# Optimization experiments

Hardware: AMD Instinct MI355X
Metric: run time of the kernel (lower is better)

The kernel has to match this reference:

```python
import jax, jax.numpy as jnp
import numpy as np

HEADS, LEVELS, POINTS, ZANCH = 8, 4, 8, 4
EMBED = 256
SHAPES = np.array([[92, 160], [46, 80], [23, 40], [12, 20]], dtype=np.int32)


def setup_inputs() -> dict:
    key = jax.random.key(0)
    k = jax.random.split(key, 9)
    bs, nq = 1, 10000
    nv = int((SHAPES[:, 0].astype(np.int64) * SHAPES[:, 1]).sum())  # 19560
    f32 = jnp.float32
    return dict(
        query=jax.random.normal(k[0], (bs, nq, EMBED), f32),
        value=jax.random.normal(k[1], (bs, nv, EMBED), f32),
        query_pos=0.1 * jax.random.normal(k[2], (bs, nq, EMBED), f32),
        reference_points=jax.random.uniform(k[3], (bs, nq, ZANCH, 2), dtype=f32),
        spatial_shapes=jnp.asarray(SHAPES),
        W_off=0.01 * jax.random.normal(k[4], (EMBED, HEADS * LEVELS * POINTS * 2), f32),
        b_off=0.5 * jax.random.normal(k[5], (HEADS * LEVELS * POINTS * 2,), f32),
        W_attn=0.01 * jax.random.normal(k[6], (EMBED, HEADS * LEVELS * POINTS), f32),
        b_attn=jnp.zeros((HEADS * LEVELS * POINTS,), f32),
        W_val=(1.0 / np.sqrt(EMBED)) * jax.random.normal(k[7], (EMBED, EMBED), f32),
        b_val=jnp.zeros((EMBED,), f32),
        W_out=(1.0 / np.sqrt(EMBED)) * jax.random.normal(k[8], (EMBED, EMBED), f32),
        b_out=jnp.zeros((EMBED,), f32),
    )


def _bilinear(v_l, x, y, Hl, Wl):
    # v_l: [bs, heads, Hl*Wl, d]; x, y: [bs, nq, heads, P] pixel coords
    # (torch grid_sample, align_corners=False, zero padding): px = loc*W - 0.5
    bs, nq, heads, P = x.shape
    d = v_l.shape[-1]
    x0 = jnp.floor(x)
    y0 = jnp.floor(y)
    lx = x - x0
    ly = y - y0
    x0i = x0.astype(jnp.int32)
    y0i = y0.astype(jnp.int32)

    def corner(xi, yi, w):
        valid = (xi >= 0) & (xi < Wl) & (yi >= 0) & (yi < Hl)
        idx = jnp.clip(yi, 0, Hl - 1) * Wl + jnp.clip(xi, 0, Wl - 1)
        idxr = idx.transpose(0, 2, 1, 3).reshape(bs, heads, nq * P)
        g = jnp.take_along_axis(v_l, idxr[..., None], axis=2)  # [bs,heads,nq*P,d]
        g = g.reshape(bs, heads, nq, P, d).transpose(0, 2, 1, 3, 4)
        return g * (w * valid.astype(w.dtype))[..., None]

    return (corner(x0i, y0i, (1 - lx) * (1 - ly))
            + corner(x0i + 1, y0i, lx * (1 - ly))
            + corner(x0i, y0i + 1, (1 - lx) * ly)
            + corner(x0i + 1, y0i + 1, lx * ly))


def reference(query, value, query_pos, reference_points, spatial_shapes,
              W_off, b_off, W_attn, b_attn, W_val, b_val, W_out, b_out):
    shapes = np.asarray(spatial_shapes)  # static per-level (H, W)
    bs, nq, E = query.shape
    heads = HEADS
    L = shapes.shape[0]
    P = W_off.shape[1] // (heads * L * 2)
    Z = reference_points.shape[2]
    d = E // heads

    residual = query
    q = query + query_pos
    v = (value @ W_val + b_val).reshape(bs, -1, heads, d)

    off = (q @ W_off + b_off).reshape(bs, nq, heads, L, P, 2)
    attn = jax.nn.softmax((q @ W_attn + b_attn).reshape(bs, nq, heads, L * P), axis=-1)
    attn = attn.reshape(bs, nq, heads, L, P)

    # normalize offsets by (W, H) per level, add Z-anchor reference points
    norm = jnp.asarray(np.stack([shapes[:, 1], shapes[:, 0]], -1), off.dtype)  # [L,2]
    off = off / norm[None, None, None, :, None, :]
    loc = (reference_points[:, :, None, None, None, :, :]
           + off.reshape(bs, nq, heads, L, P // Z, Z, 2)).reshape(bs, nq, heads, L, P, 2)

    starts = np.concatenate([[0], np.cumsum(shapes[:, 0].astype(np.int64) * shapes[:, 1])])
    out = jnp.zeros((bs, nq, heads, d), q.dtype)
    for l in range(L):  # small fixed loop over pyramid levels
        Hl, Wl = int(shapes[l, 0]), int(shapes[l, 1])
        v_l = v[:, int(starts[l]):int(starts[l + 1])].transpose(0, 2, 1, 3)  # [bs,heads,HW,d]
        x = loc[:, :, :, l, :, 0] * Wl - 0.5
        y = loc[:, :, :, l, :, 1] * Hl - 0.5
        sampled = _bilinear(v_l, x, y, Hl, Wl)  # [bs,nq,heads,P,d]
        out = out + (sampled * attn[:, :, :, l, :, None]).sum(axis=3)

    out = out.reshape(bs, nq, E) @ W_out + b_out
    return out + residual  # dropout is identity at eval
```

## Files before the change

kernel.cpp:

```cpp
#include <hip/hip_runtime.h>
#include <hip/hip_bf16.h>
#include <math.h>

typedef __hip_bfloat16 bf16;
typedef short short8_t __attribute__((ext_vector_type(8)));
typedef float f32x4 __attribute__((ext_vector_type(4)));

#define EMBED 256
#define ZANCH 4

__global__ __launch_bounds__(256) void k_prep(
    const float* __restrict__ Woff, const float* __restrict__ Wattn,
    const float* __restrict__ Wval, const float* __restrict__ Wout,
    bf16* __restrict__ wt,
    const float* __restrict__ value, bf16* __restrict__ vb,
    const float* __restrict__ query, const float* __restrict__ query_pos,
    bf16* __restrict__ qb)
{
    const int b = blockIdx.x;
    const int tid = threadIdx.x;
    if (b < 320) {
        __shared__ float tile[32][33];
        const int tn = b >> 3, tk = b & 7;
        const int r = tid >> 5, c = tid & 31;
        const int n0 = tn * 32, k0t = tk * 32;
#pragma unroll
        for (int rr = r; rr < 32; rr += 8) {
            const int k = k0t + rr;
            const int n = n0 + c;
            float val;
            if (n < 512)       val = Woff[(size_t)k * 512 + n];
            else if (n < 768)  val = Wattn[(size_t)k * 256 + (n - 512)];
            else if (n < 1024) val = Wval[(size_t)k * 256 + (n - 768)];
            else               val = Wout[(size_t)k * 256 + (n - 1024)];
            tile[rr][c] = val;
        }
        __syncthreads();
#pragma unroll
        for (int rr = r; rr < 32; rr += 8) {
            const int n = n0 + rr;
            const int k = k0t + c;
            wt[(size_t)n * 256 + k] = __float2bfloat16(tile[c][rr]);
        }
    } else if (b < 5210) {
        size_t i = ((size_t)(b - 320) * 256 + tid) * 4;
        float4 a = *(const float4*)(value + i);
        vb[i + 0] = __float2bfloat16(a.x);
        vb[i + 1] = __float2bfloat16(a.y);
        vb[i + 2] = __float2bfloat16(a.z);
        vb[i + 3] = __float2bfloat16(a.w);
    } else {
        size_t i = ((size_t)(b - 5210) * 256 + tid) * 4;
        float4 a = *(const float4*)(query + i);
        float4 p = *(const float4*)(query_pos + i);
        qb[i + 0] = __float2bfloat16(a.x + p.x);
        qb[i + 1] = __float2bfloat16(a.y + p.y);
        qb[i + 2] = __float2bfloat16(a.z + p.z);
        qb[i + 3] = __float2bfloat16(a.w + p.w);
    }
}

__global__ __launch_bounds__(256) void k_gemm_vp(
    const bf16* __restrict__ vb, const bf16* __restrict__ Btv,
    const float* __restrict__ bv, bf16* __restrict__ vhl, int Mv,
    const bf16* __restrict__ qb, const bf16* __restrict__ Btcat,
    const float* __restrict__ boff, const float* __restrict__ battn,
    float* __restrict__ raw, int Mq)
{
    __shared__ char sm[33792];
    float* smE  = (float*)sm;
    bf16*  smEv = (bf16*)sm;

    const int tid  = threadIdx.x;
    const int lane = tid & 63;
    const int wv   = tid >> 6;
    const int c16  = lane & 15, quad = lane >> 4;
    const int nwave = wv * 64;

    const bool isval = (blockIdx.y == 3);
    const int M = isval ? Mv : Mq;
    if ((int)blockIdx.x >= (M + 31) / 32) return;
    const int row0 = blockIdx.x * 32;
    const bf16* A  = isval ? vb : qb;
    const bf16* Bt = isval ? Btv : (Btcat + (size_t)(blockIdx.y * 256) * 256);

    f32x4 acc[2][4] = {};
    {
        size_t aoff[2], boffr[4];
#pragma unroll
        for (int mt = 0; mt < 2; ++mt) {
            int r = row0 + mt * 16 + c16;
            r = (r < M) ? r : (M - 1);
            aoff[mt] = (size_t)r * 256 + quad * 8;
        }
#pragma unroll
        for (int nt = 0; nt < 4; ++nt)
            boffr[nt] = (size_t)(nwave + nt * 16 + c16) * 256 + quad * 8;
#pragma unroll
        for (int k0 = 0; k0 < 256; k0 += 32) {
            short8_t a[2], b[4];
#pragma unroll
            for (int mt = 0; mt < 2; ++mt) a[mt] = *(const short8_t*)(A + aoff[mt] + k0);
#pragma unroll
            for (int nt = 0; nt < 4; ++nt) b[nt] = *(const short8_t*)(Bt + boffr[nt] + k0);
#pragma unroll
            for (int mt = 0; mt < 2; ++mt)
#pragma unroll
                for (int nt = 0; nt < 4; ++nt)
                    acc[mt][nt] = __builtin_amdgcn_mfma_f32_16x16x32_bf16(
                        a[mt], b[nt], acc[mt][nt], 0, 0, 0);
        }
    }

    if (isval) {
#pragma unroll
        for (int nt = 0; nt < 4; ++nt) {
            const int colg = nwave + nt * 16 + c16;
            const float bias = bv[colg];
#pragma unroll
            for (int mt = 0; mt < 2; ++mt)
#pragma unroll
                for (int reg = 0; reg < 4; ++reg) {
                    const int rl = mt * 16 + quad * 4 + reg;
                    smEv[rl * 264 + colg] = __float2bfloat16(acc[mt][nt][reg] + bias);
                }
        }
        __syncthreads();
#pragma unroll
        for (int sub = 0; sub < 2; ++sub) {
            const int h = wv * 2 + sub;
            bf16* dsth = vhl + (size_t)h * Mv * 32;
#pragma unroll
            for (int j = 0; j < 2; ++j) {
                const int s = j * 64 + lane;
                const int pix = s >> 2, seg = s & 3;
                const int rg = row0 + pix;
                if (rg < Mv)
                    *(short8_t*)(dsth + (size_t)rg * 32 + seg * 8) =
                        *(const short8_t*)(smEv + pix * 264 + h * 32 + seg * 8);
            }
        }
    } else {
#pragma unroll
        for (int nt = 0; nt < 4; ++nt) {
            const int colg = nwave + nt * 16 + c16;
            const int cg = blockIdx.y * 256 + colg;
            const float bias = (cg < 512) ? boff[cg] : battn[cg - 512];
#pragma unroll
            for (int mt = 0; mt < 2; ++mt)
#pragma unroll
                for (int reg = 0; reg < 4; ++reg) {
                    const int rl = mt * 16 + quad * 4 + reg;
                    smE[rl * 260 + colg] = acc[mt][nt][reg] + bias;
                }
        }
        __syncthreads();
#pragma unroll
        for (int rr = 0; rr < 8; ++rr) {
            const int rl = wv * 8 + rr;
            const int rg = row0 + rl;
            if (rg < Mq)
                *(f32x4*)(raw + (size_t)rg * 768 + blockIdx.y * 256 + lane * 4) =
                    *(const f32x4*)(smE + rl * 260 + lane * 4);
        }
    }
}

__global__ __launch_bounds__(256) void k_sample(
    const bf16* __restrict__ vhl, const float* __restrict__ raw,
    const float* __restrict__ refpts, bf16* __restrict__ outa, int nq, int nv)
{
    __shared__ int2 spr[16][132];
    const int tid = threadIdx.x;
    const int b = blockIdx.x;
    const int hp = (b & 7) >> 1;
    const int qg = ((b >> 3) << 1) + (b & 1);
    const int q0 = qg * 8;

    {
        const int lp = tid & 31;
        const int l = lp >> 3;
        const int p = lp & 7;
        const int z = p & (ZANCH - 1);
        const float Wlf = (l == 0) ? 160.f : (l == 1) ? 80.f : (l == 2) ? 40.f : 20.f;
        const float Hlf = (l == 0) ? 92.f : (l == 1) ? 46.f : (l == 2) ? 23.f : 12.f;
        const int Wli = (l == 0) ? 160 : (l == 1) ? 80 : (l == 2) ? 40 : 20;
        const int Hli = (l == 0) ? 92 : (l == 1) ? 46 : (l == 2) ? 23 : 12;
        const int Stl = (l == 0) ? 0 : (l == 1) ? 14720 : (l == 2) ? 18400 : 19320;

#pragma unroll
        for (int r = 0; r < 2; ++r) {
            const int g = r * 8 + (tid >> 5);
            const int q = q0 + (g >> 1);
            const int head = hp * 2 + (g & 1);
            const int col = head * 32 + lp;

            const float ox = raw[(size_t)q * 768 + 2 * col];
            const float oy = raw[(size_t)q * 768 + 2 * col + 1];
            const float lg = raw[(size_t)q * 768 + 512 + col];

            float m = lg;
            for (int o = 16; o > 0; o >>= 1) m = fmaxf(m, __shfl_xor(m, o, 32));
            float e = __expf(lg - m);
            float s = e;
            for (int o = 16; o > 0; o >>= 1) s += __shfl_xor(s, o, 32);
            const float aw = e / s;

            const float refx = refpts[(size_t)q * 8 + z * 2 + 0];
            const float refy = refpts[(size_t)q * 8 + z * 2 + 1];
            const float px = refx * Wlf + ox - 0.5f;
            const float py = refy * Hlf + oy - 0.5f;

            const float x0f = floorf(px), y0f = floorf(py);
            const int x0 = (int)x0f, y0 = (int)y0f;
            const float lx = px - x0f, ly = py - y0f;
            const float cw[4] = { (1.f - lx) * (1.f - ly), lx * (1.f - ly),
                                  (1.f - lx) * ly,         lx * ly };
#pragma unroll
            for (int c = 0; c < 4; ++c) {
                const int xi = x0 + (c & 1);
                const int yi = y0 + (c >> 1);
                const bool valid = (xi >= 0) && (xi < Wli) && (yi >= 0) && (yi < Hli);
                const int xc = min(max(xi, 0), Wli - 1);
                const int yc = min(max(yi, 0), Hli - 1);
                const float w = valid ? (cw[c] * aw) : 0.f;
                spr[g][c * 32 + lp] = make_int2(Stl + yc * Wli + xc, __float_as_int(w));
            }
        }
    }
    __syncthreads();

    const int qs = tid >> 5;
    const int hh = (tid >> 4) & 1;
    const int cp = tid & 15;
    const int g2 = qs * 2 + hh;
    const bf16* vbase = vhl + (size_t)(hp * 2 + hh) * nv * 32 + cp * 2;

    float acc0 = 0.f, acc1 = 0.f;
#pragma unroll 2
    for (int bb = 0; bb < 128; bb += 16) {
        int2 pr[16];
#pragma unroll
        for (int j = 0; j < 16; ++j) pr[j] = spr[g2][bb + j];
        int dv[16];
#pragma unroll
        for (int j = 0; j < 16; ++j)
            dv[j] = *(const int*)(vbase + (size_t)pr[j].x * 32);
#pragma unroll
        for (int j = 0; j < 16; ++j) {
            const float w = __int_as_float(pr[j].y);
            acc0 = fmaf(w, __int_as_float(dv[j] << 16), acc0);
            acc1 = fmaf(w, __int_as_float(dv[j] & 0xFFFF0000), acc1);
        }
    }
    __hip_bfloat162 o2;
    o2.x = __float2bfloat16(acc0);
    o2.y = __float2bfloat16(acc1);
    *(__hip_bfloat162*)(outa + (size_t)(q0 + qs) * 256 + (hp * 2 + hh) * 32 + cp * 2) = o2;
}

__global__ __launch_bounds__(256) void k_gemm_out(
    const bf16* __restrict__ outa, const bf16* __restrict__ Bto,
    const float* __restrict__ bo, const float* __restrict__ query,
    float* __restrict__ out, int M)
{
    const int row0 = blockIdx.x * 32;
    const int nwave = (threadIdx.x >> 6) * 64;
    const int lane = threadIdx.x & 63;
    const int c16 = lane & 15, quad = lane >> 4;

    f32x4 acc[2][4] = {};
    {
        size_t aoff[2], boffr[4];
#pragma unroll
        for (int mt = 0; mt < 2; ++mt) {
            int r = row0 + mt * 16 + c16;
            r = (r < M) ? r : (M - 1);
            aoff[mt] = (size_t)r * 256 + quad * 8;
        }
#pragma unroll
        for (int nt = 0; nt < 4; ++nt)
            boffr[nt] = (size_t)(nwave + nt * 16 + c16) * 256 + quad * 8;
#pragma unroll
        for (int k0 = 0; k0 < 256; k0 += 32) {
            short8_t a[2], b[4];
#pragma unroll
            for (int mt = 0; mt < 2; ++mt) a[mt] = *(const short8_t*)(outa + aoff[mt] + k0);
#pragma unroll
            for (int nt = 0; nt < 4; ++nt) b[nt] = *(const short8_t*)(Bto + boffr[nt] + k0);
#pragma unroll
            for (int mt = 0; mt < 2; ++mt)
#pragma unroll
                for (int nt = 0; nt < 4; ++nt)
                    acc[mt][nt] = __builtin_amdgcn_mfma_f32_16x16x32_bf16(
                        a[mt], b[nt], acc[mt][nt], 0, 0, 0);
        }
    }
#pragma unroll
    for (int nt = 0; nt < 4; ++nt) {
        int colg = nwave + nt * 16 + c16;
        float bias = bo[colg];
#pragma unroll
        for (int mt = 0; mt < 2; ++mt)
#pragma unroll
            for (int reg = 0; reg < 4; ++reg) {
                int row = row0 + mt * 16 + quad * 4 + reg;
                if (row < M) {
                    size_t o_ = (size_t)row * 256 + colg;
                    float fv = acc[mt][nt][reg] + bias + query[o_];
                    if (!(fv == fv) || fabsf(fv) > 1e30f) fv = 0.f;
                    out[o_] = fv;
                }
            }
    }
}

extern "C" void kernel_launch(void* const* d_in, const int* in_sizes, int n_in,
                              void* d_out, int out_size, void* d_ws, size_t ws_size,
                              hipStream_t stream)
{
    const float* query     = (const float*)d_in[0];
    const float* value     = (const float*)d_in[1];
    const float* query_pos = (const float*)d_in[2];
    const float* refpts    = (const float*)d_in[3];
    const float* Woff  = (const float*)d_in[5];
    const float* boff  = (const float*)d_in[6];
    const float* Wattn = (const float*)d_in[7];
    const float* battn = (const float*)d_in[8];
    const float* Wval  = (const float*)d_in[9];
    const float* bval  = (const float*)d_in[10];
    const float* Wout  = (const float*)d_in[11];
    const float* bout  = (const float*)d_in[12];
    float* out = (float*)d_out;

    const int nq = in_sizes[0] / EMBED;
    const int nv = in_sizes[1] / EMBED;

    char* base = (char*)d_ws;
    bf16*  wt   = (bf16*)base;
    bf16*  qb   = (bf16*)(base + 655360);
    bf16*  vb   = (bf16*)(base + 5775360);
    float* raw  = (float*)(base + 15790080);
    bf16*  outa = (bf16*)(base + 46510080);
    bf16*  vhl  = (bf16*)(base + 51630080);
    const bf16* Btcat = wt;
    const bf16* Btv   = wt + 768 * 256;
    const bf16* Bto   = wt + 1024 * 256;

    k_prep<<<7710, 256, 0, stream>>>(Woff, Wattn, Wval, Wout, wt,
                                     value, vb, query, query_pos, qb);
    k_gemm_vp<<<dim3((nv + 31) / 32, 4), 256, 0, stream>>>(vb, Btv, bval, vhl, nv,
                                                           qb, Btcat, boff, battn, raw, nq);
    k_sample<<<(nq / 8) * 4, 256, 0, stream>>>(vhl, raw, refpts, outa, nq, nv);
    k_gemm_out<<<(nq + 31) / 32, 256, 0, stream>>>(outa, Bto, bout, query, out, nq);
}
```

Before: 211.4 us.

## Pack sample index and fp16 weight into one int, widen per-thread channels

The sampling kernel now handles 16 queries per block instead of 8. Each sample's value index and attention-weighted bilinear weight are packed into a single 32-bit word: the upper 16 bits hold the index and the lower 16 hold the weight as fp16. Each thread now gathers 4 bf16 channels (8 bytes) per sample rather than 2, which halves the number of gather instructions and the shared-memory traffic per output. The trade-offs are reduced weight precision, an index limited to 16 bits (it fits because nv is 19560), a hardcoded grid size of 2504 that assumes nq=10000, and extra bounds clamping.

Measured after the change: 214.2 us. About the same (+1.3%).

```diff
diff --git a/kernel.cpp b/kernel.cpp
--- a/kernel.cpp
+++ b/kernel.cpp
@@ -1,10 +1,12 @@
 #include <hip/hip_runtime.h>
 #include <hip/hip_bf16.h>
+#include <hip/hip_fp16.h>
 #include <math.h>
 
 typedef __hip_bfloat16 bf16;
 typedef short short8_t __attribute__((ext_vector_type(8)));
 typedef float f32x4 __attribute__((ext_vector_type(4)));
+typedef int i32x4 __attribute__((ext_vector_type(4)));
 
 #define EMBED 256
 #define ZANCH 4
@@ -170,12 +172,12 @@
     const bf16* __restrict__ vhl, const float* __restrict__ raw,
     const float* __restrict__ refpts, bf16* __restrict__ outa, int nq, int nv)
 {
-    __shared__ int2 spr[16][132];
+    __shared__ int spr[32][132];
     const int tid = threadIdx.x;
     const int b = blockIdx.x;
     const int hp = (b & 7) >> 1;
     const int qg = ((b >> 3) << 1) + (b & 1);
-    const int q0 = qg * 8;
+    const int q0 = qg * 16;
 
     {
         const int lp = tid & 31;
@@ -189,14 +191,16 @@
         const int Stl = (l == 0) ? 0 : (l == 1) ? 14720 : (l == 2) ? 18400 : 19320;
 
 #pragma unroll
-        for (int r = 0; r < 2; ++r) {
+        for (int r = 0; r < 4; ++r) {
             const int g = r * 8 + (tid >> 5);
-            const int q = q0 + (g >> 1);
+            int q = q0 + (g >> 1);
+            q = (q < nq) ? q : (nq - 1);
             const int head = hp * 2 + (g & 1);
             const int col = head * 32 + lp;
 
-            const float ox = raw[(size_t)q * 768 + 2 * col];
-            const float oy = raw[(size_t)q * 768 + 2 * col + 1];
+            const float2 oxy = *(const float2*)(raw + (size_t)q * 768 + 2 * col);
+            const float ox = oxy.x;
+            const float oy = oxy.y;
             const float lg = raw[(size_t)q * 768 + 512 + col];
 
             float m = lg;
@@ -224,39 +228,54 @@
                 const int xc = min(max(xi, 0), Wli - 1);
                 const int yc = min(max(yi, 0), Hli - 1);
                 const float w = valid ? (cw[c] * aw) : 0.f;
-                spr[g][c * 32 + lp] = make_int2(Stl + yc * Wli + xc, __float_as_int(w));
+                const int idx = Stl + yc * Wli + xc;
+                const unsigned hw = (unsigned)__half_as_ushort(__float2half(w));
+                spr[g][c * 32 + lp] = (idx << 16) | (int)hw;
             }
         }
     }
     __syncthreads();
 
-    const int qs = tid >> 5;
-    const int hh = (tid >> 4) & 1;
-    const int cp = tid & 15;
-    const int g2 = qs * 2 + hh;
-    const bf16* vbase = vhl + (size_t)(hp * 2 + hh) * nv * 32 + cp * 2;
-
-    float acc0 = 0.f, acc1 = 0.f;
+    const int g2  = tid >> 3;
+    const int qs  = g2 >> 1;
+    const int hh  = g2 & 1;
+    const int ch4 = tid & 7;
+    const char* hpb = (const char*)vhl + (size_t)(hp * 2) * nv * 64;
+    const unsigned tb = (unsigned)(hh * nv) * 64u + (unsigned)ch4 * 8u;
+
+    float a0 = 0.f, a1 = 0.f, a2 = 0.f, a3 = 0.f;
 #pragma unroll 2
     for (int bb = 0; bb < 128; bb += 16) {
-        int2 pr[16];
-#pragma unroll
-        for (int j = 0; j < 16; ++j) pr[j] = spr[g2][bb + j];
-        int dv[16];
+        i32x4 pk4[4];
+#pragma unroll
+        for (int j = 0; j < 4; ++j) pk4[j] = *(const i32x4*)&spr[g2][bb + j * 4];
+        int pk[16];
+#pragma unroll
+        for (int j = 0; j < 16; ++j) pk[j] = pk4[j >> 2][j & 3];
+        int2 dv[16];
 #pragma unroll
         for (int j = 0; j < 16; ++j)
-            dv[j] = *(const int*)(vbase + (size_t)pr[j].x * 32);
+            dv[j] = *(const int2*)(hpb + (size_t)(tb + (((unsigned)pk[j] >> 16) << 6)));
 #pragma unroll
         for (int j = 0; j < 16; ++j) {
-            const float w = __int_as_float(pr[j].y);
-            acc0 = fmaf(w, __int_as_float(dv[j] << 16), acc0);
-            acc1 = fmaf(w, __int_as_float(dv[j] & 0xFFFF0000), acc1);
-        }
-    }
-    __hip_bfloat162 o2;
-    o2.x = __float2bfloat16(acc0);
-    o2.y = __float2bfloat16(acc1);
-    *(__hip_bfloat162*)(outa + (size_t)(q0 + qs) * 256 + (hp * 2 + hh) * 32 + cp * 2) = o2;
+            const float w = __half2float(__ushort_as_half((unsigned short)(pk[j] & 0xFFFF)));
+            a0 = fmaf(w, __int_as_float(dv[j].x << 16), a0);
+            a1 = fmaf(w, __int_as_float(dv[j].x & 0xFFFF0000), a1);
+            a2 = fmaf(w, __int_as_float(dv[j].y << 16), a2);
+            a3 = fmaf(w, __int_as_float(dv[j].y & 0xFFFF0000), a3);
+        }
+    }
+    const int qf = q0 + qs;
+    if (qf < nq) {
+        __hip_bfloat162 p01, p23;
+        p01.x = __float2bfloat16(a0);
+        p01.y = __float2bfloat16(a1);
+        p23.x = __float2bfloat16(a2);
+        p23.y = __float2bfloat16(a3);
+        bf16* dst = outa + (size_t)qf * 256 + (hp * 2 + hh) * 32 + ch4 * 4;
+        *(__hip_bfloat162*)dst = p01;
+        *(__hip_bfloat162*)(dst + 2) = p23;
+    }
 }
 
 __global__ __launch_bounds__(256) void k_gemm_out(
@@ -351,6 +370,6 @@
                                      value, vb, query, query_pos, qb);
     k_gemm_vp<<<dim3((nv + 31) / 32, 4), 256, 0, stream>>>(vb, Btv, bval, vhl, nv,
                                                            qb, Btcat, boff, battn, raw, nq);
-    k_sample<<<(nq / 8) * 4, 256, 0, stream>>>(vhl, raw, refpts, outa, nq, nv);
+    k_sample<<<2504, 256, 0, stream>>>(vhl, raw, refpts, outa, nq, nv);
     k_gemm_out<<<(nq + 31) / 32, 256, 0, stream>>>(outa, Bto, bout, query, out, nq);
 }
```

## Store projection logits in fp16 and pack sample index and weight into one int

Applied to the files above, without the earlier changes.

The offset and attention projection output is now written as fp16 instead of fp32, which halves the raw buffer traffic between the projection GEMM and the sampling kernel. In the sampling kernel, each corner's value index and bilinear-times-attention weight are packed into a single 32-bit word (16-bit index, fp16 weight) in shared memory and read back as 128-bit vector loads. The aim is to cut global and LDS bandwidth and address arithmetic. The risks are reduced precision on offsets, logits and weights, and a 16-bit index field that only holds because nv is 19560.

Result: faster. 206.8 us (-2.2%).

```diff
diff --git a/kernel.cpp b/kernel.cpp
--- a/kernel.cpp
+++ b/kernel.cpp
@@ -1,10 +1,12 @@
 #include <hip/hip_runtime.h>
 #include <hip/hip_bf16.h>
+#include <hip/hip_fp16.h>
 #include <math.h>
 
 typedef __hip_bfloat16 bf16;
 typedef short short8_t __attribute__((ext_vector_type(8)));
 typedef float f32x4 __attribute__((ext_vector_type(4)));
+typedef int i32x4 __attribute__((ext_vector_type(4)));
 
 #define EMBED 256
 #define ZANCH 4
@@ -65,7 +67,7 @@
     const float* __restrict__ bv, bf16* __restrict__ vhl, int Mv,
     const bf16* __restrict__ qb, const bf16* __restrict__ Btcat,
     const float* __restrict__ boff, const float* __restrict__ battn,
-    float* __restrict__ raw, int Mq)
+    __half* __restrict__ raw, int Mq)
 {
     __shared__ char sm[33792];
     float* smE  = (float*)sm;
@@ -159,18 +161,24 @@
         for (int rr = 0; rr < 8; ++rr) {
             const int rl = wv * 8 + rr;
             const int rg = row0 + rl;
-            if (rg < Mq)
-                *(f32x4*)(raw + (size_t)rg * 768 + blockIdx.y * 256 + lane * 4) =
-                    *(const f32x4*)(smE + rl * 260 + lane * 4);
+            if (rg < Mq) {
+                f32x4 v = *(const f32x4*)(smE + rl * 260 + lane * 4);
+                union { int2 i2; __half h[4]; } u;
+                u.h[0] = __float2half(v[0]);
+                u.h[1] = __float2half(v[1]);
+                u.h[2] = __float2half(v[2]);
+                u.h[3] = __float2half(v[3]);
+                *(int2*)(raw + (size_t)rg * 768 + blockIdx.y * 256 + lane * 4) = u.i2;
+            }
         }
     }
 }
 
 __global__ __launch_bounds__(256) void k_sample(
-    const bf16* __restrict__ vhl, const float* __restrict__ raw,
+    const bf16* __restrict__ vhl, const __half* __restrict__ raw,
     const float* __restrict__ refpts, bf16* __restrict__ outa, int nq, int nv)
 {
-    __shared__ int2 spr[16][132];
+    __shared__ int spr[16][132];
     const int tid = threadIdx.x;
     const int b = blockIdx.x;
     const int hp = (b & 7) >> 1;
@@ -195,9 +203,10 @@
             const int head = hp * 2 + (g & 1);
             const int col = head * 32 + lp;
 
-            const float ox = raw[(size_t)q * 768 + 2 * col];
-            const float oy = raw[(size_t)q * 768 + 2 * col + 1];
-            const float lg = raw[(size_t)q * 768 + 512 + col];
+            const __half2 oxy = *(const __half2*)(raw + (size_t)q * 768 + 2 * col);
+            const float ox = __half2float(oxy.x);
+            const float oy = __half2float(oxy.y);
+            const float lg = __half2float(raw[(size_t)q * 768 + 512 + col]);
 
             float m = lg;
             for (int o = 16; o > 0; o >>= 1) m = fmaxf(m, __shfl_xor(m, o, 32));
@@ -224,38 +233,43 @@
                 const int xc = min(max(xi, 0), Wli - 1);
                 const int yc = min(max(yi, 0), Hli - 1);
                 const float w = valid ? (cw[c] * aw) : 0.f;
-                spr[g][c * 32 + lp] = make_int2(Stl + yc * Wli + xc, __float_as_int(w));
+                const int idx = Stl + yc * Wli + xc;
+                const unsigned hw = (unsigned)__half_as_ushort(__float2half(w));
+                spr[g][c * 32 + lp] = (idx << 16) | (int)hw;
             }
         }
     }
     __syncthreads();
 
-    const int qs = tid >> 5;
-    const int hh = (tid >> 4) & 1;
-    const int cp = tid & 15;
-    const int g2 = qs * 2 + hh;
-    const bf16* vbase = vhl + (size_t)(hp * 2 + hh) * nv * 32 + cp * 2;
-
-    float acc0 = 0.f, acc1 = 0.f;
+    const int g2  = tid >> 4;
+    const int qs  = g2 >> 1;
+    const int hh  = g2 & 1;
+    const int cp  = tid & 15;
+    const char* hpb = (const char*)vhl + (size_t)(hp * 2) * nv * 64;
+    const unsigned tbase = (unsigned)(hh * nv) * 64u + (unsigned)cp * 4u;
+
+    float a0 = 0.f, a1 = 0.f;
 #pragma unroll 2
     for (int bb = 0; bb < 128; bb += 16) {
-        int2 pr[16];
-#pragma unroll
-        for (int j = 0; j < 16; ++j) pr[j] = spr[g2][bb + j];
+        i32x4 pk4[4];
+#pragma unroll
+        for (int j = 0; j < 4; ++j) pk4[j] = *(const i32x4*)&spr[g2][bb + j * 4];
         int dv[16];
 #pragma unroll
         for (int j = 0; j < 16; ++j)
-            dv[j] = *(const int*)(vbase + (size_t)pr[j].x * 32);
+            dv[j] = *(const int*)(hpb +
+                (size_t)(tbase + (((unsigned)pk4[j >> 2][j & 3] >> 16) << 6)));
 #pragma unroll
         for (int j = 0; j < 16; ++j) {
-            const float w = __int_as_float(pr[j].y);
-            acc0 = fmaf(w, __int_as_float(dv[j] << 16), acc0);
-            acc1 = fmaf(w, __int_as_float(dv[j] & 0xFFFF0000), acc1);
+            const int pkj = pk4[j >> 2][j & 3];
+            const float w = __half2float(__ushort_as_half((unsigned short)(pkj & 0xFFFF)));
+            a0 = fmaf(w, __int_as_float(dv[j] << 16), a0);
+            a1 = fmaf(w, __int_as_float(dv[j] & 0xFFFF0000), a1);
         }
     }
     __hip_bfloat162 o2;
-    o2.x = __float2bfloat16(acc0);
-    o2.y = __float2bfloat16(acc1);
+    o2.x = __float2bfloat16(a0);
+    o2.y = __float2bfloat16(a1);
     *(__hip_bfloat162*)(outa + (size_t)(q0 + qs) * 256 + (hp * 2 + hh) * 32 + cp * 2) = o2;
 }
 
@@ -337,12 +351,12 @@
     const int nv = in_sizes[1] / EMBED;
 
     char* base = (char*)d_ws;
-    bf16*  wt   = (bf16*)base;
-    bf16*  qb   = (bf16*)(base + 655360);
-    bf16*  vb   = (bf16*)(base + 5775360);
-    float* raw  = (float*)(base + 15790080);
-    bf16*  outa = (bf16*)(base + 46510080);
-    bf16*  vhl  = (bf16*)(base + 51630080);
+    bf16*   wt   = (bf16*)base;
+    bf16*   qb   = (bf16*)(base + 655360);
+    bf16*   vb   = (bf16*)(base + 5775360);
+    __half* raw  = (__half*)(base + 15790080);
+    bf16*   outa = (bf16*)(base + 31150080);
+    bf16*   vhl  = (bf16*)(base + 36270080);
     const bf16* Btcat = wt;
     const bf16* Btv   = wt + 768 * 256;
     const bf16* Bto   = wt + 1024 * 256;
```
